# Performance work log

Hardware: AMD Instinct MI355X
Metric: run time of the kernel (lower is better)

The kernel has to match this reference:

```python
import jax, jax.numpy as jnp
import numpy as np

VOCAB = 50000
E = 32            # embed_size; node state is E x E
LABELS = 10
DEPTH = 11        # perfect binary tree: 2^DEPTH - 1 = 2047 nodes, 1024 leaves
N_NODES = 2 ** DEPTH - 1
LN_EPS = 1e-5


def setup_inputs() -> dict:
    key = jax.random.key(0)
    ks = jax.random.split(key, 8)
    word_ids = jax.random.randint(ks[0], (N_NODES,), 0, VOCAB, dtype=jnp.int32)
    label = 3
    emb_table = jax.random.normal(ks[1], (VOCAB, E * E), dtype=jnp.float32) * 0.02
    Ww = jax.random.normal(ks[2], (E, E), dtype=jnp.float32) * (1.0 / np.sqrt(E))
    Wb = jax.random.normal(ks[3], (E,), dtype=jnp.float32) * 0.01
    gamma = jnp.ones((E, E), dtype=jnp.float32)   # LayerNorm((1,E,E)) affine weight
    beta = jnp.zeros((E, E), dtype=jnp.float32)
    Pw = jax.random.normal(ks[4], (LABELS, E * E), dtype=jnp.float32) * (1.0 / E)
    Pb = jnp.zeros((LABELS,), dtype=jnp.float32)
    return {"word_ids": word_ids, "label": label, "emb_table": emb_table,
            "Ww": Ww, "Wb": Wb, "gamma": gamma, "beta": beta, "Pw": Pw, "Pb": Pb}


def reference(word_ids, label, emb_table, Ww, Wb, gamma, beta, Pw, Pb):
    # word_ids: level-order ids of a perfect binary tree, children of within-level
    # index j at level d are indices 2j, 2j+1 at level d+1.
    embs = emb_table[word_ids].reshape(N_NODES, E, E)  # [N, E, E]

    def ln_relu(x):
        # torch LayerNorm((1,E,E)): normalize over the whole E*E matrix, affine per element
        mu = jnp.mean(x, axis=(1, 2), keepdims=True)
        var = jnp.var(x, axis=(1, 2), keepdims=True)
        y = (x - mu) * jax.lax.rsqrt(var + LN_EPS) * gamma + beta
        return jax.nn.relu(y)

    # leaves: level DEPTH-1
    start = 2 ** (DEPTH - 1) - 1
    h = ln_relu(embs[start:])  # [2^(DEPTH-1), E, E]
    # internal levels bottom-up; loop over fixed DEPTH-1 levels (not data dims)
    for d in range(DEPTH - 2, -1, -1):
        s = 2 ** d - 1
        cur = embs[s:s + 2 ** d]                     # [n_d, E, E]
        l, r = h[0::2], h[1::2]                      # children pairs
        x = jnp.einsum('nij,njk,nkl->nil', l, r, cur)
        x = x @ Ww.T + Wb                            # Linear applied row-wise
        h = ln_relu(x)

    root = h[0].reshape(-1)                          # [E*E]
    logits = root @ Pw.T + Pb                        # [LABELS]
    prediction = jnp.argmax(logits)
    loss = -jax.nn.log_softmax(logits)[label]
    return (prediction, loss)
```

## Files before the change

### kernel.cpp

```cpp
#include <hip/hip_runtime.h>
#include <hip/hip_bf16.h>

#define LN_EPS 1e-5f
#define TSB 40
#define TILEB (32 * TSB)

typedef __attribute__((ext_vector_type(8))) short bf16x8;
typedef __attribute__((ext_vector_type(16))) float f32x16;

__device__ __forceinline__ short bf16b(float f) {
  return __builtin_bit_cast(short, __float2bfloat16(f));
}

__device__ __forceinline__ void wave_reduce2(float& s1, float& s2) {
  #pragma unroll
  for (int off = 32; off; off >>= 1) {
    s1 += __shfl_xor(s1, off);
    s2 += __shfl_xor(s2, off);
  }
}

__device__ __forceinline__ bf16x8 frag_ld(const short* t, int l, int k0) {
  return *(const bf16x8*)&t[(l & 31) * TSB + ((l >> 5) << 3) + k0];
}

__device__ __forceinline__ int cd_row(int r, int l) {
  return (r & 3) + 8 * (r >> 2) + 4 * (l >> 5);
}

__device__ __forceinline__ void cd_store(short* t, int l, const f32x16 d,
                                         bool transp) {
  const int col = l & 31;
  if (transp) {
    #pragma unroll
    for (int r = 0; r < 16; ++r) t[col * TSB + cd_row(r, l)] = bf16b(d[r]);
  } else {
    #pragma unroll
    for (int r = 0; r < 16; ++r) t[cd_row(r, l) * TSB + col] = bf16b(d[r]);
  }
}

struct NodeParams {
  bf16x8 w0, w1;
  float wb;
  float ga[16], be[16];
};

__device__ __forceinline__ NodeParams load_params(const float* __restrict__ Ww,
    const float* __restrict__ Wb, const float* __restrict__ gamma,
    const float* __restrict__ beta, int l) {
  NodeParams P;
  const int n = l & 31, kh = (l >> 5) * 8;
  float w[8];
  *(float4*)&w[0] = *(const float4*)&Ww[n * 32 + kh];
  *(float4*)&w[4] = *(const float4*)&Ww[n * 32 + kh + 4];
  #pragma unroll
  for (int i = 0; i < 8; ++i) P.w0[i] = bf16b(w[i]);
  *(float4*)&w[0] = *(const float4*)&Ww[n * 32 + kh + 16];
  *(float4*)&w[4] = *(const float4*)&Ww[n * 32 + kh + 20];
  #pragma unroll
  for (int i = 0; i < 8; ++i) P.w1[i] = bf16b(w[i]);
  P.wb = Wb[n];
  #pragma unroll
  for (int r = 0; r < 16; ++r) {
    const int idx = cd_row(r, l) * 32 + n;
    P.ga[r] = gamma[idx];
    P.be[r] = beta[idx];
  }
  return P;
}

__device__ __forceinline__ f32x16 mm32(const short* A, const short* B, int l) {
  f32x16 acc = {};
  acc = __builtin_amdgcn_mfma_f32_32x32x16_bf16(frag_ld(A, l, 0),
                                                frag_ld(B, l, 0), acc, 0, 0, 0);
  acc = __builtin_amdgcn_mfma_f32_32x32x16_bf16(frag_ld(A, l, 16),
                                                frag_ld(B, l, 16), acc, 0, 0, 0);
  return acc;
}

__device__ __forceinline__ void node_mfma(short* A, short* Bt, const short* Ct,
                                          const NodeParams& P, int l,
                                          short* dst, bool transpOut,
                                          float* fout) {
  f32x16 t1 = mm32(A, Bt, l);
  cd_store(A, l, t1, false);
  f32x16 t2 = mm32(A, Ct, l);
  cd_store(Bt, l, t2, false);
  f32x16 x = {};
  x = __builtin_amdgcn_mfma_f32_32x32x16_bf16(frag_ld(Bt, l, 0), P.w0, x, 0, 0, 0);
  x = __builtin_amdgcn_mfma_f32_32x32x16_bf16(frag_ld(Bt, l, 16), P.w1, x, 0, 0, 0);
  float s1 = 0.f, s2 = 0.f;
  #pragma unroll
  for (int r = 0; r < 16; ++r) {
    x[r] += P.wb;
    s1 += x[r];
    s2 += x[r] * x[r];
  }
  wave_reduce2(s1, s2);
  const float mu = s1 * (1.f / 1024.f);
  const float rs = rsqrtf(s2 * (1.f / 1024.f) - mu * mu + LN_EPS);
  #pragma unroll
  for (int r = 0; r < 16; ++r)
    x[r] = fmaxf((x[r] - mu) * rs * P.ga[r] + P.be[r], 0.f);
  if (fout) {
    #pragma unroll
    for (int r = 0; r < 16; ++r) fout[cd_row(r, l) * 32 + (l & 31)] = x[r];
  } else {
    cd_store(dst, l, x, transpOut);
  }
}

__device__ __forceinline__ void stage_f32(short* dst,
                                          const float* __restrict__ src, int l,
                                          bool transp) {
  float v[16];
  #pragma unroll
  for (int q = 0; q < 4; ++q)
    *(float4*)&v[q * 4] = *(const float4*)&src[l * 16 + q * 4];
  const int row = l >> 1, c0 = (l & 1) * 16;
  if (transp) {
    #pragma unroll
    for (int i = 0; i < 16; ++i) dst[(c0 + i) * TSB + row] = bf16b(v[i]);
  } else {
    #pragma unroll
    for (int i = 0; i < 8; ++i) {
      unsigned lo = (unsigned short)bf16b(v[2 * i]);
      unsigned hi = (unsigned short)bf16b(v[2 * i + 1]);
      ((unsigned*)dst)[row * (TSB / 2) + (c0 >> 1) + i] = lo | (hi << 16);
    }
  }
}

__device__ __forceinline__ void stage_bf16(short* dst,
                                           const short* __restrict__ src, int l,
                                           bool transp) {
  short v[16];
  *(bf16x8*)&v[0] = *(const bf16x8*)&src[l * 16];
  *(bf16x8*)&v[8] = *(const bf16x8*)&src[l * 16 + 8];
  const int row = l >> 1, c0 = (l & 1) * 16;
  if (transp) {
    #pragma unroll
    for (int i = 0; i < 16; ++i) dst[(c0 + i) * TSB + row] = v[i];
  } else {
    #pragma unroll
    for (int i = 0; i < 8; ++i) {
      unsigned lo = (unsigned short)v[2 * i];
      unsigned hi = (unsigned short)v[2 * i + 1];
      ((unsigned*)dst)[row * (TSB / 2) + (c0 >> 1) + i] = lo | (hi << 16);
    }
  }
}

__device__ __forceinline__ void copy_out(short* __restrict__ dst, const short* t,
                                         int u) {
  if (u < 128) {
    const int row = u >> 2, c0 = (u & 3) * 8;
    *(bf16x8*)&dst[row * 32 + c0] = *(const bf16x8*)&t[row * TSB + c0];
  }
}

__device__ __forceinline__ void leaf_ln(short* dst, const float* __restrict__ src,
                                        const float* __restrict__ gamma,
                                        const float* __restrict__ beta, int l,
                                        bool transp) {
  float v[16], ga[16], be[16];
  #pragma unroll
  for (int q = 0; q < 4; ++q) {
    *(float4*)&v[q * 4] = *(const float4*)&src[l * 16 + q * 4];
    *(float4*)&ga[q * 4] = *(const float4*)&gamma[l * 16 + q * 4];
    *(float4*)&be[q * 4] = *(const float4*)&beta[l * 16 + q * 4];
  }
  float s1 = 0.f, s2 = 0.f;
  #pragma unroll
  for (int i = 0; i < 16; ++i) { s1 += v[i]; s2 += v[i] * v[i]; }
  wave_reduce2(s1, s2);
  const float mu = s1 * (1.f / 1024.f);
  const float rs = rsqrtf(s2 * (1.f / 1024.f) - mu * mu + LN_EPS);
  #pragma unroll
  for (int i = 0; i < 16; ++i)
    v[i] = fmaxf((v[i] - mu) * rs * ga[i] + be[i], 0.f);
  const int row = l >> 1, c0 = (l & 1) * 16;
  if (transp) {
    #pragma unroll
    for (int i = 0; i < 16; ++i) dst[(c0 + i) * TSB + row] = bf16b(v[i]);
  } else {
    #pragma unroll
    for (int i = 0; i < 8; ++i) {
      unsigned lo = (unsigned short)bf16b(v[2 * i]);
      unsigned hi = (unsigned short)bf16b(v[2 * i + 1]);
      ((unsigned*)dst)[row * (TSB / 2) + (c0 >> 1) + i] = lo | (hi << 16);
    }
  }
}

__global__ __launch_bounds__(512) void k_bot7(
    const int* __restrict__ wid, const float* __restrict__ emb,
    const float* __restrict__ Ww, const float* __restrict__ Wb,
    const float* __restrict__ gamma, const float* __restrict__ beta,
    short* __restrict__ h7) {
  __shared__ __align__(16) short pool[15 * TILEB];
  const int u = threadIdx.x, blk = blockIdx.x;
  const int wv = u >> 6, l = u & 63;
  NodeParams P = load_params(Ww, Wb, gamma, beta, l);
  if (wv < 4)
    stage_f32(pool + (8 + wv) * TILEB,
              emb + (size_t)wid[511 + 4 * blk + wv] * 1024, l, true);
  else if (wv < 6)
    stage_f32(pool + (8 + wv) * TILEB,
              emb + (size_t)wid[255 + 2 * blk + (wv - 4)] * 1024, l, true);
  else if (wv == 6)
    stage_f32(pool + 14 * TILEB, emb + (size_t)wid[127 + blk] * 1024, l, true);
  leaf_ln(pool + wv * TILEB, emb + (size_t)wid[1023 + 8 * blk + wv] * 1024,
          gamma, beta, l, (wv & 1) != 0);
  __syncthreads();
  if (wv < 4)
    node_mfma(pool + 2 * wv * TILEB, pool + (2 * wv + 1) * TILEB,
              pool + (8 + wv) * TILEB, P, l, pool + (8 + wv) * TILEB,
              (wv & 1) != 0, nullptr);
  __syncthreads();
  if (wv < 2)
    node_mfma(pool + (8 + 2 * wv) * TILEB, pool + (9 + 2 * wv) * TILEB,
              pool + (12 + wv) * TILEB, P, l, pool + (12 + wv) * TILEB,
              (wv & 1) != 0, nullptr);
  __syncthreads();
  if (wv == 0)
    node_mfma(pool + 12 * TILEB, pool + 13 * TILEB, pool + 14 * TILEB, P, l,
              pool + 14 * TILEB, false, nullptr);
  __syncthreads();
  copy_out(h7 + (size_t)blk * 1024, pool + 14 * TILEB, u);
}

__global__ __launch_bounds__(512) void k_mid16(
    const int* __restrict__ wid, const float* __restrict__ emb,
    const float* __restrict__ Ww, const float* __restrict__ Wb,
    const float* __restrict__ gamma, const float* __restrict__ beta,
    const short* __restrict__ hin, short* __restrict__ hout) {
  __shared__ __align__(16) short pool[15 * TILEB];
  const int u = threadIdx.x, blk = blockIdx.x;
  const int wv = u >> 6, l = u & 63;
  NodeParams P = load_params(Ww, Wb, gamma, beta, l);
  stage_bf16(pool + wv * TILEB, hin + (size_t)(8 * blk + wv) * 1024, l,
             (wv & 1) != 0);
  if (wv < 4)
    stage_f32(pool + (8 + wv) * TILEB,
              emb + (size_t)wid[63 + 4 * blk + wv] * 1024, l, true);
  else if (wv < 6)
    stage_f32(pool + (8 + wv) * TILEB,
              emb + (size_t)wid[31 + 2 * blk + (wv - 4)] * 1024, l, true);
  else if (wv == 6)
    stage_f32(pool + 14 * TILEB, emb + (size_t)wid[15 + blk] * 1024, l, true);
  __syncthreads();
  if (wv < 4)
    node_mfma(pool + 2 * wv * TILEB, pool + (2 * wv + 1) * TILEB,
              pool + (8 + wv) * TILEB, P, l, pool + (8 + wv) * TILEB,
              (wv & 1) != 0, nullptr);
  __syncthreads();
  if (wv < 2)
    node_mfma(pool + (8 + 2 * wv) * TILEB, pool + (9 + 2 * wv) * TILEB,
              pool + (12 + wv) * TILEB, P, l, pool + (12 + wv) * TILEB,
              (wv & 1) != 0, nullptr);
  __syncthreads();
  if (wv == 0)
    node_mfma(pool + 12 * TILEB, pool + 13 * TILEB, pool + 14 * TILEB, P, l,
              pool + 14 * TILEB, false, nullptr);
  __syncthreads();
  copy_out(hout + (size_t)blk * 1024, pool + 14 * TILEB, u);
}

__global__ __launch_bounds__(512) void k_top2(
    const int* __restrict__ wid, const float* __restrict__ emb,
    const float* __restrict__ Ww, const float* __restrict__ Wb,
    const float* __restrict__ gamma, const float* __restrict__ beta,
    const float* __restrict__ Pw, const float* __restrict__ Pb,
    const int* __restrict__ label, const short* __restrict__ hin,
    float* __restrict__ out) {
  __shared__ __align__(16) short pool[31 * TILEB];
  __shared__ float rootf[1024];
  __shared__ float lred[10];
  const int u = threadIdx.x;
  const int wv = u >> 6, l = u & 63;
  NodeParams P = load_params(Ww, Wb, gamma, beta, l);
  stage_bf16(pool + 2 * wv * TILEB, hin + (size_t)(2 * wv) * 1024, l, false);
  stage_bf16(pool + (2 * wv + 1) * TILEB, hin + (size_t)(2 * wv + 1) * 1024, l,
             true);
  stage_f32(pool + (16 + wv) * TILEB, emb + (size_t)wid[7 + wv] * 1024, l, true);
  if (wv < 4)
    stage_f32(pool + (24 + wv) * TILEB, emb + (size_t)wid[3 + wv] * 1024, l, true);
  else if (wv < 6)
    stage_f32(pool + (24 + wv) * TILEB,
              emb + (size_t)wid[1 + (wv - 4)] * 1024, l, true);
  else if (wv == 6)
    stage_f32(pool + 30 * TILEB, emb + (size_t)wid[0] * 1024, l, true);
  __syncthreads();
  node_mfma(pool + 2 * wv * TILEB, pool + (2 * wv + 1) * TILEB,
            pool + (16 + wv) * TILEB, P, l, pool + (16 + wv) * TILEB,
            (wv & 1) != 0, nullptr);
  __syncthreads();
  if (wv < 4)
    node_mfma(pool + (16 + 2 * wv) * TILEB, pool + (17 + 2 * wv) * TILEB,
              pool + (24 + wv) * TILEB, P, l, pool + (24 + wv) * TILEB,
              (wv & 1) != 0, nullptr);
  __syncthreads();
  if (wv < 2)
    node_mfma(pool + (24 + 2 * wv) * TILEB, pool + (25 + 2 * wv) * TILEB,
              pool + (28 + wv) * TILEB, P, l, pool + (28 + wv) * TILEB,
              (wv & 1) != 0, nullptr);
  __syncthreads();
  if (wv == 0)
    node_mfma(pool + 28 * TILEB, pool + 29 * TILEB, pool + 30 * TILEB, P, l,
              nullptr, false, rootf);
  __syncthreads();
  #pragma unroll
  for (int q = 0; q < 2; ++q) {
    const int c = wv + 8 * q;
    if (c < 10) {
      float p = 0.f;
      #pragma unroll
      for (int t = 0; t < 4; ++t) {
        float4 r4 = *(const float4*)&rootf[l * 16 + t * 4];
        float4 w4 = *(const float4*)&Pw[c * 1024 + l * 16 + t * 4];
        p += r4.x * w4.x + r4.y * w4.y + r4.z * w4.z + r4.w * w4.w;
      }
      #pragma unroll
      for (int off = 32; off; off >>= 1) p += __shfl_xor(p, off);
      if (l == 0) lred[c] = p + Pb[c];
    }
  }
  __syncthreads();
  if (u == 0) {
    float mmax = lred[0];
    int am = 0;
    #pragma unroll
    for (int c = 1; c < 10; ++c)
      if (lred[c] > mmax) { mmax = lred[c]; am = c; }
    float sum = 0.f;
    #pragma unroll
    for (int c = 0; c < 10; ++c) sum += expf(lred[c] - mmax);
    const float loss = -(lred[label[0]] - mmax - logf(sum));
    out[0] = (float)am;
    out[1] = loss;
  }
}

extern "C" void kernel_launch(void* const* d_in, const int* in_sizes, int n_in,
                              void* d_out, int out_size, void* d_ws, size_t ws_size,
                              hipStream_t stream) {
  const int* wid = (const int*)d_in[0];
  const int* label = (const int*)d_in[1];
  const float* emb = (const float*)d_in[2];
  const float* Ww = (const float*)d_in[3];
  const float* Wb = (const float*)d_in[4];
  const float* g = (const float*)d_in[5];
  const float* b = (const float*)d_in[6];
  const float* Pw = (const float*)d_in[7];
  const float* Pb = (const float*)d_in[8];
  float* out = (float*)d_out;

  short* h7 = (short*)d_ws;
  short* h4 = h7 + 128 * 1024;

  k_bot7<<<128, 512, 0, stream>>>(wid, emb, Ww, Wb, g, b, h7);
  k_mid16<<<16, 512, 0, stream>>>(wid, emb, Ww, Wb, g, b, h7, h4);
  k_top2<<<1, 512, 0, stream>>>(wid, emb, Ww, Wb, g, b, Pw, Pb, label, h4, out);
}
```

Baseline: 30.55 us.

## Precompute cur·Wᵀ per node off the critical path and fold linear into chain

Uses associativity: (L·R·C)·Wᵀ = L·R·(C·Wᵀ), so each node's embedding is multiplied by Wᵀ during staging, before the dependency chain starts. The per-level critical path then shrinks from three dependent 32x32 matmuls to two. The change also vectorizes the transposed bf16 store, and in the top kernel it runs the first level right after each wave's own staging, removing one barrier. The extra bf16 rounding of C·Wᵀ slightly changes numerics, and the staging waves now do more MFMA work up front.

```diff
diff --git a/kernel.cpp b/kernel.cpp
--- a/kernel.cpp
+++ b/kernel.cpp
@@ -6,6 +6,7 @@
 #define TILEB (32 * TSB)
 
 typedef __attribute__((ext_vector_type(8))) short bf16x8;
+typedef __attribute__((ext_vector_type(4))) short s16x4;
 typedef __attribute__((ext_vector_type(16))) float f32x16;
 
 __device__ __forceinline__ short bf16b(float f) {
@@ -28,13 +29,25 @@
   return (r & 3) + 8 * (r >> 2) + 4 * (l >> 5);
 }
 
+__device__ __forceinline__ void cd_store_t(short* t, int l, const f32x16 d) {
+  const int col = l & 31, h4 = 4 * (l >> 5);
+  #pragma unroll
+  for (int q = 0; q < 4; ++q) {
+    s16x4 p;
+    p[0] = bf16b(d[4 * q + 0]);
+    p[1] = bf16b(d[4 * q + 1]);
+    p[2] = bf16b(d[4 * q + 2]);
+    p[3] = bf16b(d[4 * q + 3]);
+    *(s16x4*)&t[col * TSB + 8 * q + h4] = p;
+  }
+}
+
 __device__ __forceinline__ void cd_store(short* t, int l, const f32x16 d,
                                          bool transp) {
-  const int col = l & 31;
   if (transp) {
-    #pragma unroll
-    for (int r = 0; r < 16; ++r) t[col * TSB + cd_row(r, l)] = bf16b(d[r]);
-  } else {
+    cd_store_t(t, l, d);
+  } else {
+    const int col = l & 31;
     #pragma unroll
     for (int r = 0; r < 16; ++r) t[cd_row(r, l) * TSB + col] = bf16b(d[r]);
   }
@@ -79,38 +92,6 @@
   return acc;
 }
 
-__device__ __forceinline__ void node_mfma(short* A, short* Bt, const short* Ct,
-                                          const NodeParams& P, int l,
-                                          short* dst, bool transpOut,
-                                          float* fout) {
-  f32x16 t1 = mm32(A, Bt, l);
-  cd_store(A, l, t1, false);
-  f32x16 t2 = mm32(A, Ct, l);
-  cd_store(Bt, l, t2, false);
-  f32x16 x = {};
-  x = __builtin_amdgcn_mfma_f32_32x32x16_bf16(frag_ld(Bt, l, 0), P.w0, x, 0, 0, 0);
-  x = __builtin_amdgcn_mfma_f32_32x32x16_bf16(frag_ld(Bt, l, 16), P.w1, x, 0, 0, 0);
-  float s1 = 0.f, s2 = 0.f;
-  #pragma unroll
-  for (int r = 0; r < 16; ++r) {
-    x[r] += P.wb;
-    s1 += x[r];
-    s2 += x[r] * x[r];
-  }
-  wave_reduce2(s1, s2);
-  const float mu = s1 * (1.f / 1024.f);
-  const float rs = rsqrtf(s2 * (1.f / 1024.f) - mu * mu + LN_EPS);
-  #pragma unroll
-  for (int r = 0; r < 16; ++r)
-    x[r] = fmaxf((x[r] - mu) * rs * P.ga[r] + P.be[r], 0.f);
-  if (fout) {
-    #pragma unroll
-    for (int r = 0; r < 16; ++r) fout[cd_row(r, l) * 32 + (l & 31)] = x[r];
-  } else {
-    cd_store(dst, l, x, transpOut);
-  }
-}
-
 __device__ __forceinline__ void stage_f32(short* dst,
                                           const float* __restrict__ src, int l,
                                           bool transp) {
@@ -129,6 +110,43 @@
       unsigned hi = (unsigned short)bf16b(v[2 * i + 1]);
       ((unsigned*)dst)[row * (TSB / 2) + (c0 >> 1) + i] = lo | (hi << 16);
     }
+  }
+}
+
+__device__ __forceinline__ void cw_prep(short* slot,
+                                        const float* __restrict__ src,
+                                        const NodeParams& P, int l) {
+  stage_f32(slot, src, l, false);
+  f32x16 cw = {};
+  cw = __builtin_amdgcn_mfma_f32_32x32x16_bf16(frag_ld(slot, l, 0), P.w0, cw, 0, 0, 0);
+  cw = __builtin_amdgcn_mfma_f32_32x32x16_bf16(frag_ld(slot, l, 16), P.w1, cw, 0, 0, 0);
+  cd_store_t(slot, l, cw);
+}
+
+__device__ __forceinline__ void node2(short* A, short* Bt, short* CWt,
+                                      const NodeParams& P, int l, short* dst,
+                                      bool transpOut, float* fout) {
+  f32x16 t1 = mm32(A, Bt, l);
+  cd_store(A, l, t1, false);
+  f32x16 x = mm32(A, CWt, l);
+  float s1 = 0.f, s2 = 0.f;
+  #pragma unroll
+  for (int r = 0; r < 16; ++r) {
+    x[r] += P.wb;
+    s1 += x[r];
+    s2 += x[r] * x[r];
+  }
+  wave_reduce2(s1, s2);
+  const float mu = s1 * (1.f / 1024.f);
+  const float rs = rsqrtf(s2 * (1.f / 1024.f) - mu * mu + LN_EPS);
+  #pragma unroll
+  for (int r = 0; r < 16; ++r)
+    x[r] = fmaxf((x[r] - mu) * rs * P.ga[r] + P.be[r], 0.f);
+  if (fout) {
+    #pragma unroll
+    for (int r = 0; r < 16; ++r) fout[cd_row(r, l) * 32 + (l & 31)] = x[r];
+  } else {
+    cd_store(dst, l, x, transpOut);
   }
 }
 
@@ -177,18 +195,19 @@
   wave_reduce2(s1, s2);
   const float mu = s1 * (1.f / 1024.f);
   const float rs = rsqrtf(s2 * (1.f / 1024.f) - mu * mu + LN_EPS);
+  float o[16];
   #pragma unroll
   for (int i = 0; i < 16; ++i)
-    v[i] = fmaxf((v[i] - mu) * rs * ga[i] + be[i], 0.f);
+    o[i] = fmaxf((v[i] - mu) * rs * ga[i] + be[i], 0.f);
   const int row = l >> 1, c0 = (l & 1) * 16;
   if (transp) {
     #pragma unroll
-    for (int i = 0; i < 16; ++i) dst[(c0 + i) * TSB + row] = bf16b(v[i]);
+    for (int i = 0; i < 16; ++i) dst[(c0 + i) * TSB + row] = bf16b(o[i]);
   } else {
     #pragma unroll
     for (int i = 0; i < 8; ++i) {
-      unsigned lo = (unsigned short)bf16b(v[2 * i]);
-      unsigned hi = (unsigned short)bf16b(v[2 * i + 1]);
+      unsigned lo = (unsigned short)bf16b(o[2 * i]);
+      unsigned hi = (unsigned short)bf16b(o[2 * i + 1]);
       ((unsigned*)dst)[row * (TSB / 2) + (c0 >> 1) + i] = lo | (hi << 16);
     }
   }
@@ -203,30 +222,30 @@
   const int u = threadIdx.x, blk = blockIdx.x;
   const int wv = u >> 6, l = u & 63;
   NodeParams P = load_params(Ww, Wb, gamma, beta, l);
-  if (wv < 4)
-    stage_f32(pool + (8 + wv) * TILEB,
-              emb + (size_t)wid[511 + 4 * blk + wv] * 1024, l, true);
-  else if (wv < 6)
-    stage_f32(pool + (8 + wv) * TILEB,
-              emb + (size_t)wid[255 + 2 * blk + (wv - 4)] * 1024, l, true);
-  else if (wv == 6)
-    stage_f32(pool + 14 * TILEB, emb + (size_t)wid[127 + blk] * 1024, l, true);
   leaf_ln(pool + wv * TILEB, emb + (size_t)wid[1023 + 8 * blk + wv] * 1024,
           gamma, beta, l, (wv & 1) != 0);
-  __syncthreads();
-  if (wv < 4)
-    node_mfma(pool + 2 * wv * TILEB, pool + (2 * wv + 1) * TILEB,
-              pool + (8 + wv) * TILEB, P, l, pool + (8 + wv) * TILEB,
-              (wv & 1) != 0, nullptr);
+  if (wv < 4)
+    cw_prep(pool + (8 + wv) * TILEB,
+            emb + (size_t)wid[511 + 4 * blk + wv] * 1024, P, l);
+  else if (wv < 6)
+    cw_prep(pool + (8 + wv) * TILEB,
+            emb + (size_t)wid[255 + 2 * blk + (wv - 4)] * 1024, P, l);
+  else if (wv == 6)
+    cw_prep(pool + 14 * TILEB, emb + (size_t)wid[127 + blk] * 1024, P, l);
+  __syncthreads();
+  if (wv < 4)
+    node2(pool + 2 * wv * TILEB, pool + (2 * wv + 1) * TILEB,
+          pool + (8 + wv) * TILEB, P, l, pool + (8 + wv) * TILEB,
+          (wv & 1) != 0, nullptr);
   __syncthreads();
   if (wv < 2)
-    node_mfma(pool + (8 + 2 * wv) * TILEB, pool + (9 + 2 * wv) * TILEB,
-              pool + (12 + wv) * TILEB, P, l, pool + (12 + wv) * TILEB,
-              (wv & 1) != 0, nullptr);
+    node2(pool + (8 + 2 * wv) * TILEB, pool + (9 + 2 * wv) * TILEB,
+          pool + (12 + wv) * TILEB, P, l, pool + (12 + wv) * TILEB,
+          (wv & 1) != 0, nullptr);
   __syncthreads();
   if (wv == 0)
-    node_mfma(pool + 12 * TILEB, pool + 13 * TILEB, pool + 14 * TILEB, P, l,
-              pool + 14 * TILEB, false, nullptr);
+    node2(pool + 12 * TILEB, pool + 13 * TILEB, pool + 14 * TILEB, P, l,
+          pool + 14 * TILEB, false, nullptr);
   __syncthreads();
   copy_out(h7 + (size_t)blk * 1024, pool + 14 * TILEB, u);
 }
@@ -243,27 +262,27 @@
   stage_bf16(pool + wv * TILEB, hin + (size_t)(8 * blk + wv) * 1024, l,
              (wv & 1) != 0);
   if (wv < 4)
-    stage_f32(pool + (8 + wv) * TILEB,
-              emb + (size_t)wid[63 + 4 * blk + wv] * 1024, l, true);
+    cw_prep(pool + (8 + wv) * TILEB,
+            emb + (size_t)wid[63 + 4 * blk + wv] * 1024, P, l);
   else if (wv < 6)
-    stage_f32(pool + (8 + wv) * TILEB,
-              emb + (size_t)wid[31 + 2 * blk + (wv - 4)] * 1024, l, true);
+    cw_prep(pool + (8 + wv) * TILEB,
+            emb + (size_t)wid[31 + 2 * blk + (wv - 4)] * 1024, P, l);
   else if (wv == 6)
-    stage_f32(pool + 14 * TILEB, emb + (size_t)wid[15 + blk] * 1024, l, true);
-  __syncthreads();
-  if (wv < 4)
-    node_mfma(pool + 2 * wv * TILEB, pool + (2 * wv + 1) * TILEB,
-              pool + (8 + wv) * TILEB, P, l, pool + (8 + wv) * TILEB,
-              (wv & 1) != 0, nullptr);
+    cw_prep(pool + 14 * TILEB, emb + (size_t)wid[15 + blk] * 1024, P, l);
+  __syncthreads();
+  if (wv < 4)
+    node2(pool + 2 * wv * TILEB, pool + (2 * wv + 1) * TILEB,
+          pool + (8 + wv) * TILEB, P, l, pool + (8 + wv) * TILEB,
+          (wv & 1) != 0, nullptr);
   __syncthreads();
   if (wv < 2)
-    node_mfma(pool + (8 + 2 * wv) * TILEB, pool + (9 + 2 * wv) * TILEB,
-              pool + (12 + wv) * TILEB, P, l, pool + (12 + wv) * TILEB,
-              (wv & 1) != 0, nullptr);
+    node2(pool + (8 + 2 * wv) * TILEB, pool + (9 + 2 * wv) * TILEB,
+          pool + (12 + wv) * TILEB, P, l, pool + (12 + wv) * TILEB,
+          (wv & 1) != 0, nullptr);
   __syncthreads();
   if (wv == 0)
-    node_mfma(pool + 12 * TILEB, pool + 13 * TILEB, pool + 14 * TILEB, P, l,
-              pool + 14 * TILEB, false, nullptr);
+    node2(pool + 12 * TILEB, pool + 13 * TILEB, pool + 14 * TILEB, P, l,
+          pool + 14 * TILEB, false, nullptr);
   __syncthreads();
   copy_out(hout + (size_t)blk * 1024, pool + 14 * TILEB, u);
 }
@@ -284,32 +303,31 @@
   stage_bf16(pool + 2 * wv * TILEB, hin + (size_t)(2 * wv) * 1024, l, false);
   stage_bf16(pool + (2 * wv + 1) * TILEB, hin + (size_t)(2 * wv + 1) * 1024, l,
              true);
-  stage_f32(pool + (16 + wv) * TILEB, emb + (size_t)wid[7 + wv] * 1024, l, true);
-  if (wv < 4)
-    stage_f32(pool + (24 + wv) * TILEB, emb + (size_t)wid[3 + wv] * 1024, l, true);
+  cw_prep(pool + (16 + wv) * TILEB, emb + (size_t)wid[7 + wv] * 1024, P, l);
+  node2(pool + 2 * wv * TILEB, pool + (2 * wv + 1) * TILEB,
+        pool + (16 + wv) * TILEB, P, l, pool + (16 + wv) * TILEB,
+        (wv & 1) != 0, nullptr);
+  if (wv < 4)
+    cw_prep(pool + (24 + wv) * TILEB, emb + (size_t)wid[3 + wv] * 1024, P, l);
   else if (wv < 6)
-    stage_f32(pool + (24 + wv) * TILEB,
-              emb + (size_t)wid[1 + (wv - 4)] * 1024, l, true);
+    cw_prep(pool + (28 + (wv - 4)) * TILEB,
+            emb + (size_t)wid[1 + (wv - 4)] * 1024, P, l);
   else if (wv == 6)
-    stage_f32(pool + 30 * TILEB, emb + (size_t)wid[0] * 1024, l, true);
-  __syncthreads();
-  node_mfma(pool + 2 * wv * TILEB, pool + (2 * wv + 1) * TILEB,
-            pool + (16 + wv) * TILEB, P, l, pool + (16 + wv) * TILEB,
-            (wv & 1) != 0, nullptr);
-  __syncthreads();
-  if (wv < 4)
-    node_mfma(pool + (16 + 2 * wv) * TILEB, pool + (17 + 2 * wv) * TILEB,
-              pool + (24 + wv) * TILEB, P, l, pool + (24 + wv) * TILEB,
-              (wv & 1) != 0, nullptr);
+    cw_prep(pool + 30 * TILEB, emb + (size_t)wid[0] * 1024, P, l);
+  __syncthreads();
+  if (wv < 4)
+    node2(pool + (16 + 2 * wv) * TILEB, pool + (17 + 2 * wv) * TILEB,
+          pool + (24 + wv) * TILEB, P, l, pool + (24 + wv) * TILEB,
+          (wv & 1) != 0, nullptr);
   __syncthreads();
   if (wv < 2)
-    node_mfma(pool + (24 + 2 * wv) * TILEB, pool + (25 + 2 * wv) * TILEB,
-              pool + (28 + wv) * TILEB, P, l, pool + (28 + wv) * TILEB,
-              (wv & 1) != 0, nullptr);
+    node2(pool + (24 + 2 * wv) * TILEB, pool + (25 + 2 * wv) * TILEB,
+          pool + (28 + wv) * TILEB, P, l, pool + (28 + wv) * TILEB,
+          (wv & 1) != 0, nullptr);
   __syncthreads();
   if (wv == 0)
-    node_mfma(pool + 28 * TILEB, pool + 29 * TILEB, pool + 30 * TILEB, P, l,
-              nullptr, false, rootf);
+    node2(pool + 28 * TILEB, pool + 29 * TILEB, pool + 30 * TILEB, P, l,
+          nullptr, false, rootf);
   __syncthreads();
   #pragma unroll
   for (int q = 0; q < 2; ++q) {
```

Measured after the change: 28.11 us. -8.0%, faster.
